# Optimization experiments

Measured on AMD Instinct MI355X. Metric: run time of the kernel, lower is better.

Reference implementation:

```python
import jax, jax.numpy as jnp
import numpy as np

BLOCK = 64


def setup_inputs() -> dict:
    key = jax.random.key(0)
    k1, k2, k3, k4 = jax.random.split(key, 4)
    B, K, N = 32, 4096, 14336
    x = jax.random.normal(k1, (B, K), dtype=jnp.float32)
    # int8-range quantized weights stored as int32 for portability
    qweight = jax.random.randint(k2, (N, K), -127, 128, dtype=jnp.int32)
    # per-block scales, fp16 like the torch module
    scales = (jax.random.uniform(k3, (N, K // BLOCK), dtype=jnp.float32) * 0.02 + 1e-4).astype(jnp.float16)
    bias = jax.random.normal(k4, (N,), dtype=jnp.float32)
    return {"x": x, "qweight": qweight, "scales": scales, "bias": bias}


def reference(x, qweight, scales, bias):
    # Blockwise dequant: w[n, b*64+j] = qweight[n, b*64+j] * scales[n, b]
    N, K = qweight.shape
    nb = K // BLOCK
    w = (qweight.astype(x.dtype).reshape(N, nb, BLOCK)
         * scales.astype(x.dtype)[:, :, None]).reshape(N, K)
    # out[b, n] = sum_k x[b, k] * w[n, k]  (sum over all K blocks, fused)
    out = jnp.einsum('bk,nk->bn', x, w) + bias.astype(x.dtype)
    return out
```

## Files before the change

### kernel.cpp

```cpp
#include <hip/hip_runtime.h>
#include <hip/hip_bf16.h>
#include <hip/hip_fp16.h>

#define K_DIM 4096
#define N_DIM 14336
#define B_M   32
#define NSTEPS 128
#define NTILES (N_DIM / 16)
#define WAVES 4
#define WCHUNKS 16

typedef __attribute__((ext_vector_type(8))) short short8;
typedef __attribute__((ext_vector_type(4))) float f32x4;
typedef __attribute__((ext_vector_type(4))) int   i32x4;

static __device__ __forceinline__ short f2bf(float f) {
    union { float f; unsigned u; } v; v.f = f;
    unsigned r = v.u + 0x7FFFu + ((v.u >> 16) & 1u);
    return (short)(r >> 16);
}

__global__ __launch_bounds__(256) void prep_xa_kernel(const float* __restrict__ x,
                                                      short* __restrict__ xa) {
    int t2 = blockIdx.x * 256 + threadIdx.x;
    int l = t2 & 63;
    int f = (t2 >> 6) & 1;
    int s = t2 >> 7;
    int m = 16 * f + (l & 15);
    int k = 32 * s + 8 * (l >> 4);
    const float* src = x + (size_t)m * K_DIM + k;
    f32x4 v0 = *(const f32x4*)(src);
    f32x4 v1 = *(const f32x4*)(src + 4);
    short8 o;
    #pragma unroll
    for (int j = 0; j < 4; ++j) { o[j] = f2bf(v0[j]); o[j + 4] = f2bf(v1[j]); }
    *(short8*)(xa + (size_t)t2 * 8) = o;
}

__global__ __launch_bounds__(256, 4) void gemm_lds_kernel(
        const int* __restrict__ qw, const short* __restrict__ xa,
        const float* __restrict__ scales, const float* __restrict__ bias,
        float* __restrict__ out) {
    __shared__ int lds2[2][4096];

    const int tid  = threadIdx.x;
    const int w    = tid >> 6;
    const int lane = tid & 63;
    const int g    = lane >> 4;
    const int nl   = lane & 15;
    const int n0   = blockIdx.x * 16;
    const int n    = n0 + nl;
    const int gc0  = w * WCHUNKS;

    const float* srow = scales + (size_t)n * (K_DIM / 64);

    auto stage = [&](int* wbuf, int gc) {
        #pragma unroll
        for (int i = 0; i < 4; ++i) {
            int row = i * 4 + (lane >> 4);
            int l   = (lane & 15) ^ (row & 7);
            const int* src = qw + (size_t)(n0 + row) * K_DIM + gc * 64 + l * 4;
            __builtin_amdgcn_global_load_lds(
                (const __attribute__((address_space(1))) void*)src,
                (__attribute__((address_space(3))) void*)(wbuf + i * 256),
                16, 0, 0);
        }
    };

    auto loada = [&](short8 (&ar)[4], int gc) {
        const short* base = xa + (size_t)(gc * 2) * 1024 + lane * 8;
        ar[0] = *(const short8*)(base);
        ar[1] = *(const short8*)(base + 512);
        ar[2] = *(const short8*)(base + 1024);
        ar[3] = *(const short8*)(base + 1536);
    };

    f32x4 acc0 = {0.f, 0.f, 0.f, 0.f};
    f32x4 acc1 = {0.f, 0.f, 0.f, 0.f};

    auto compute = [&](const int* wbuf, const short8 (&ar)[4], float sc) {
        const int base = nl * 64;
        #pragma unroll
        for (int sp = 0; sp < 2; ++sp) {
            int uA = 8 * sp + 2 * g;
            i32x4 qa = *(const i32x4*)(wbuf + base + ((uA    ) ^ (nl & 7)) * 4);
            i32x4 qb = *(const i32x4*)(wbuf + base + ((uA + 1) ^ (nl & 7)) * 4);

            short8 a0 = ar[2 * sp];
            short8 a1 = ar[2 * sp + 1];

            short8 bw;
            bw[0] = f2bf((float)qa[0] * sc);
            bw[1] = f2bf((float)qa[1] * sc);
            bw[2] = f2bf((float)qa[2] * sc);
            bw[3] = f2bf((float)qa[3] * sc);
            bw[4] = f2bf((float)qb[0] * sc);
            bw[5] = f2bf((float)qb[1] * sc);
            bw[6] = f2bf((float)qb[2] * sc);
            bw[7] = f2bf((float)qb[3] * sc);

            acc0 = __builtin_amdgcn_mfma_f32_16x16x32_bf16(a0, bw, acc0, 0, 0, 0);
            acc1 = __builtin_amdgcn_mfma_f32_16x16x32_bf16(a1, bw, acc1, 0, 0, 0);
        }
    };

    f32x4 s4[4];
    #pragma unroll
    for (int i = 0; i < 4; ++i) s4[i] = *(const f32x4*)(srow + gc0 + i * 4);
    asm volatile("s_waitcnt vmcnt(0)" ::: "memory");

    short8 aE[4], aO[4];

    stage(lds2[0] + w * 1024, gc0 + 0);
    loada(aE, gc0 + 0);

    #pragma unroll
    for (int c = 0; c < WCHUNKS; ++c) {
        if (c + 1 < WCHUNKS) {
            stage(lds2[(c + 1) & 1] + w * 1024, gc0 + c + 1);
            if (c & 1) loada(aE, gc0 + c + 1); else loada(aO, gc0 + c + 1);
        }
        if (c < WCHUNKS - 1) {
            asm volatile("s_waitcnt vmcnt(8)" ::: "memory");
        } else {
            asm volatile("s_waitcnt vmcnt(0)" ::: "memory");
        }

        const int*  wbuf = lds2[c & 1] + w * 1024;
        const float sc   = s4[c >> 2][c & 3];
        if (c & 1) compute(wbuf, aO, sc); else compute(wbuf, aE, sc);
    }

    float* fb = (float*)(lds2[0] + w * 1024);
    #pragma unroll
    for (int r = 0; r < 4; ++r) { fb[lane * 9 + r] = acc0[r]; fb[lane * 9 + 4 + r] = acc1[r]; }
    __syncthreads();

    const int lane2 = tid & 63;
    const int rr    = tid >> 6;
    const int g2    = lane2 >> 4;
    const int n2    = n0 + (lane2 & 15);
    float s1 = 0.f, s2 = 0.f;
    #pragma unroll
    for (int ww = 0; ww < WAVES; ++ww) {
        const float* fw = (const float*)(lds2[0] + ww * 1024);
        s1 += fw[lane2 * 9 + rr];
        s2 += fw[lane2 * 9 + 4 + rr];
    }
    const float bv = bias[n2];
    out[(size_t)(4 * g2 + rr) * N_DIM + n2]      = s1 + bv;
    out[(size_t)(16 + 4 * g2 + rr) * N_DIM + n2] = s2 + bv;
}

__global__ __launch_bounds__(64) void gemm_reg_kernel(
        const int* __restrict__ qw, const float* __restrict__ x,
        const float* __restrict__ scales, const float* __restrict__ bias,
        float* __restrict__ out) {
    const int lane = threadIdx.x;
    const int g = lane >> 4, nl = lane & 15;
    const int n = blockIdx.x * 16 + nl;
    const int* qrow = qw + (size_t)n * K_DIM + 8 * g;
    const float* srow = scales + (size_t)n * (K_DIM / 64);
    const float* xr0 = x + (size_t)nl * K_DIM + 8 * g;
    const float* xr1 = xr0 + (size_t)16 * K_DIM;
    f32x4 acc0 = {0.f,0.f,0.f,0.f}, acc1 = {0.f,0.f,0.f,0.f};
    for (int s = 0; s < NSTEPS; ++s) {
        i32x4 qa = *(const i32x4*)(qrow + 32 * s);
        i32x4 qb = *(const i32x4*)(qrow + 32 * s + 4);
        float sc = srow[s >> 1];
        f32x4 x00 = *(const f32x4*)(xr0 + 32 * s), x01 = *(const f32x4*)(xr0 + 32 * s + 4);
        f32x4 x10 = *(const f32x4*)(xr1 + 32 * s), x11 = *(const f32x4*)(xr1 + 32 * s + 4);
        short8 a0, a1, bw;
        #pragma unroll
        for (int j = 0; j < 4; ++j) { a0[j]=f2bf(x00[j]); a0[j+4]=f2bf(x01[j]);
                                      a1[j]=f2bf(x10[j]); a1[j+4]=f2bf(x11[j]);
                                      bw[j]=f2bf((float)qa[j]*sc); bw[j+4]=f2bf((float)qb[j]*sc); }
        acc0 = __builtin_amdgcn_mfma_f32_16x16x32_bf16(a0, bw, acc0, 0, 0, 0);
        acc1 = __builtin_amdgcn_mfma_f32_16x16x32_bf16(a1, bw, acc1, 0, 0, 0);
    }
    float bv = bias[n];
    float* pp = out + n;
    #pragma unroll
    for (int r = 0; r < 4; ++r) {
        pp[(size_t)(4 * g + r) * N_DIM]      = acc0[r] + bv;
        pp[(size_t)(16 + 4 * g + r) * N_DIM] = acc1[r] + bv;
    }
}

extern "C" void kernel_launch(void* const* d_in, const int* in_sizes, int n_in,
                              void* d_out, int out_size, void* d_ws, size_t ws_size,
                              hipStream_t stream) {
    const float* x    = (const float*)d_in[0];
    const int*   qw   = (const int*)d_in[1];
    const float* sc   = (const float*)d_in[2];
    const float* bias = (const float*)d_in[3];
    float* out = (float*)d_out;

    const size_t XA_BYTES = (size_t)B_M * K_DIM * 2;

    if (ws_size >= XA_BYTES) {
        short* xa = (short*)d_ws;
        prep_xa_kernel<<<dim3(64), dim3(256), 0, stream>>>(x, xa);
        gemm_lds_kernel<<<dim3(NTILES), dim3(256), 0, stream>>>(qw, xa, sc, bias, out);
    } else {
        gemm_reg_kernel<<<dim3(NTILES), dim3(64), 0, stream>>>(qw, x, sc, bias, out);
    }
}
```

Before: 45.67 us.

## Give each wave its own N tile over full K instead of split-K reduction

Each workgroup now covers 64 output columns, with each wave owning 16 columns and looping over the full K dimension in 128-wide chunks. Before, four waves split K for 16 columns and combined partial sums through LDS. Dropping the split removes the cross-wave LDS reduction and the barrier, and doubling the chunk size halves the number of loop iterations. In exchange the grid has 224 blocks instead of 896, so each wave runs a longer serial chain, occupancy drops, and there may be too few waves to keep the memory system saturated.

```diff
diff --git a/kernel.cpp b/kernel.cpp
--- a/kernel.cpp
+++ b/kernel.cpp
@@ -6,12 +6,12 @@
 #define N_DIM 14336
 #define B_M   32
 #define NSTEPS 128
-#define NTILES (N_DIM / 16)
-#define WAVES 4
-#define WCHUNKS 16
+#define CHUNKS32 32
+#define NBLOCKS (N_DIM / 64)
 
 typedef __attribute__((ext_vector_type(8))) short short8;
 typedef __attribute__((ext_vector_type(4))) float f32x4;
+typedef __attribute__((ext_vector_type(2))) float f32x2;
 typedef __attribute__((ext_vector_type(4))) int   i32x4;
 
 static __device__ __forceinline__ short f2bf(float f) {
@@ -37,29 +37,28 @@
     *(short8*)(xa + (size_t)t2 * 8) = o;
 }
 
-__global__ __launch_bounds__(256, 4) void gemm_lds_kernel(
+__global__ __launch_bounds__(256, 2) void gemm_lds_kernel(
         const int* __restrict__ qw, const short* __restrict__ xa,
         const float* __restrict__ scales, const float* __restrict__ bias,
         float* __restrict__ out) {
-    __shared__ int lds2[2][4096];
+    __shared__ int lds2[2][4][2048];
 
     const int tid  = threadIdx.x;
     const int w    = tid >> 6;
     const int lane = tid & 63;
     const int g    = lane >> 4;
     const int nl   = lane & 15;
-    const int n0   = blockIdx.x * 16;
-    const int n    = n0 + nl;
-    const int gc0  = w * WCHUNKS;
+    const int nw   = blockIdx.x * 64 + w * 16;
+    const int n    = nw + nl;
 
     const float* srow = scales + (size_t)n * (K_DIM / 64);
 
     auto stage = [&](int* wbuf, int gc) {
         #pragma unroll
-        for (int i = 0; i < 4; ++i) {
-            int row = i * 4 + (lane >> 4);
-            int l   = (lane & 15) ^ (row & 7);
-            const int* src = qw + (size_t)(n0 + row) * K_DIM + gc * 64 + l * 4;
+        for (int i = 0; i < 8; ++i) {
+            int row = 2 * i + (lane >> 5);
+            int u   = (lane & 31) ^ (row & 7);
+            const int* src = qw + (size_t)(nw + row) * K_DIM + gc * 128 + u * 4;
             __builtin_amdgcn_global_load_lds(
                 (const __attribute__((address_space(1))) void*)src,
                 (__attribute__((address_space(3))) void*)(wbuf + i * 256),
@@ -67,21 +66,23 @@
         }
     };
 
-    auto loada = [&](short8 (&ar)[4], int gc) {
-        const short* base = xa + (size_t)(gc * 2) * 1024 + lane * 8;
-        ar[0] = *(const short8*)(base);
-        ar[1] = *(const short8*)(base + 512);
-        ar[2] = *(const short8*)(base + 1024);
-        ar[3] = *(const short8*)(base + 1536);
+    auto loada = [&](short8 (&ar)[8], int gc) {
+        const short* base = xa + (size_t)(gc * 4) * 1024 + lane * 8;
+        #pragma unroll
+        for (int s = 0; s < 4; ++s) {
+            ar[2 * s]     = *(const short8*)(base + s * 1024);
+            ar[2 * s + 1] = *(const short8*)(base + s * 1024 + 512);
+        }
     };
 
     f32x4 acc0 = {0.f, 0.f, 0.f, 0.f};
     f32x4 acc1 = {0.f, 0.f, 0.f, 0.f};
 
-    auto compute = [&](const int* wbuf, const short8 (&ar)[4], float sc) {
-        const int base = nl * 64;
+    auto compute = [&](const int* wbuf, const short8 (&ar)[8], f32x2 scp) {
+        const int base = nl * 128;
         #pragma unroll
-        for (int sp = 0; sp < 2; ++sp) {
+        for (int sp = 0; sp < 4; ++sp) {
+            const float sc = (sp < 2) ? scp[0] : scp[1];
             int uA = 8 * sp + 2 * g;
             i32x4 qa = *(const i32x4*)(wbuf + base + ((uA    ) ^ (nl & 7)) * 4);
             i32x4 qb = *(const i32x4*)(wbuf + base + ((uA + 1) ^ (nl & 7)) * 4);
@@ -104,52 +105,37 @@
         }
     };
 
-    f32x4 s4[4];
-    #pragma unroll
-    for (int i = 0; i < 4; ++i) s4[i] = *(const f32x4*)(srow + gc0 + i * 4);
-    asm volatile("s_waitcnt vmcnt(0)" ::: "memory");
+    short8 aE[8], aO[8];
+    f32x2  scE, scO;
 
-    short8 aE[4], aO[4];
-
-    stage(lds2[0] + w * 1024, gc0 + 0);
-    loada(aE, gc0 + 0);
+    stage(&lds2[0][w][0], 0);
+    loada(aE, 0);
+    scE = *(const f32x2*)(srow);
 
     #pragma unroll
-    for (int c = 0; c < WCHUNKS; ++c) {
-        if (c + 1 < WCHUNKS) {
-            stage(lds2[(c + 1) & 1] + w * 1024, gc0 + c + 1);
-            if (c & 1) loada(aE, gc0 + c + 1); else loada(aO, gc0 + c + 1);
+    for (int c = 0; c < CHUNKS32; ++c) {
+        if (c + 1 < CHUNKS32) {
+            stage(&lds2[(c + 1) & 1][w][0], c + 1);
+            if (c & 1) { loada(aE, c + 1); scE = *(const f32x2*)(srow + 2 * (c + 1)); }
+            else       { loada(aO, c + 1); scO = *(const f32x2*)(srow + 2 * (c + 1)); }
         }
-        if (c < WCHUNKS - 1) {
-            asm volatile("s_waitcnt vmcnt(8)" ::: "memory");
+        if (c < CHUNKS32 - 1) {
+            asm volatile("s_waitcnt vmcnt(17)" ::: "memory");
         } else {
             asm volatile("s_waitcnt vmcnt(0)" ::: "memory");
         }
 
-        const int*  wbuf = lds2[c & 1] + w * 1024;
-        const float sc   = s4[c >> 2][c & 3];
-        if (c & 1) compute(wbuf, aO, sc); else compute(wbuf, aE, sc);
+        const int* wbuf = &lds2[c & 1][w][0];
+        if (c & 1) compute(wbuf, aO, scO); else compute(wbuf, aE, scE);
     }
 
-    float* fb = (float*)(lds2[0] + w * 1024);
+    const float bv = bias[n];
+    float* pp = out + n;
     #pragma unroll
-    for (int r = 0; r < 4; ++r) { fb[lane * 9 + r] = acc0[r]; fb[lane * 9 + 4 + r] = acc1[r]; }
-    __syncthreads();
-
-    const int lane2 = tid & 63;
-    const int rr    = tid >> 6;
-    const int g2    = lane2 >> 4;
-    const int n2    = n0 + (lane2 & 15);
-    float s1 = 0.f, s2 = 0.f;
-    #pragma unroll
-    for (int ww = 0; ww < WAVES; ++ww) {
-        const float* fw = (const float*)(lds2[0] + ww * 1024);
-        s1 += fw[lane2 * 9 + rr];
-        s2 += fw[lane2 * 9 + 4 + rr];
+    for (int r = 0; r < 4; ++r) {
+        pp[(size_t)(4 * g + r) * N_DIM]      = acc0[r] + bv;
+        pp[(size_t)(16 + 4 * g + r) * N_DIM] = acc1[r] + bv;
     }
-    const float bv = bias[n2];
-    out[(size_t)(4 * g2 + rr) * N_DIM + n2]      = s1 + bv;
-    out[(size_t)(16 + 4 * g2 + rr) * N_DIM + n2] = s2 + bv;
 }
 
 __global__ __launch_bounds__(64) void gemm_reg_kernel(
@@ -201,8 +187,8 @@
     if (ws_size >= XA_BYTES) {
         short* xa = (short*)d_ws;
         prep_xa_kernel<<<dim3(64), dim3(256), 0, stream>>>(x, xa);
-        gemm_lds_kernel<<<dim3(NTILES), dim3(256), 0, stream>>>(qw, xa, sc, bias, out);
+        gemm_lds_kernel<<<dim3(NBLOCKS), dim3(256), 0, stream>>>(qw, xa, sc, bias, out);
     } else {
-        gemm_reg_kernel<<<dim3(NTILES), dim3(64), 0, stream>>>(qw, x, sc, bias, out);
+        gemm_reg_kernel<<<dim3(N_DIM / 16), dim3(64), 0, stream>>>(qw, x, sc, bias, out);
     }
 }
```

Measured after the change: 51.53 us. +12.8%, slower.
